# Kernel tuning notes

Hardware: AMD Instinct MI355X
Metric: run time of the kernel (lower is better)

The kernel has to match this reference:

```python
import jax, jax.numpy as jnp
import numpy as np

B, H, W, C = 16, 32, 32, 512
L, CT = 77, 512
NH, HD = 8, 64
G = 32          # GroupNorm groups
EPS = 1e-6      # flax GroupNorm default epsilon
NEG = -1e10


def group_norm(x, scale, bias):
    # flax GroupNorm on [b, n, c]: stats over (n, channels-within-group) per (b, group)
    b, n, c = x.shape
    xg = x.reshape(b, n, G, c // G)
    mu = xg.mean(axis=(1, 3), keepdims=True)
    var = xg.var(axis=(1, 3), keepdims=True)
    xg = (xg - mu) * jax.lax.rsqrt(var + EPS)
    return xg.reshape(b, n, c) * scale + bias


def setup_inputs() -> dict:
    key = jax.random.key(0)
    ks = jax.random.split(key, 8)
    w = lambda k, shape: jax.random.normal(k, shape, jnp.float32) * 0.02
    return {
        "inputs": jax.random.normal(ks[0], (B, H, W, C), jnp.float32),
        "text_enc": jax.random.normal(ks[1], (B, L, CT), jnp.float32),
        "text_mask": jnp.ones((B, L), jnp.int32),
        "gn_q_scale": jnp.ones((C,), jnp.float32),
        "gn_q_bias": jnp.zeros((C,), jnp.float32),
        "gn_kv_scale": jnp.ones((C,), jnp.float32),
        "gn_kv_bias": jnp.zeros((C,), jnp.float32),
        "gn_t_scale": jnp.ones((CT,), jnp.float32),
        "gn_t_bias": jnp.zeros((CT,), jnp.float32),
        "Wq": w(ks[2], (C, NH, HD)),
        "Wk_self": w(ks[3], (C, NH, HD)),
        "Wv_self": w(ks[4], (C, NH, HD)),
        "Wk_cross": w(ks[5], (CT, NH, HD)),
        "Wv_cross": w(ks[6], (CT, NH, HD)),
        "Wout": w(ks[7], (NH, HD, C)),
    }


def reference(inputs, text_enc, text_mask,
              gn_q_scale, gn_q_bias, gn_kv_scale, gn_kv_bias,
              gn_t_scale, gn_t_bias,
              Wq, Wk_self, Wv_self, Wk_cross, Wv_cross, Wout):
    b, h, w, c = inputs.shape
    n = h * w
    x = inputs.reshape(b, n, c)

    x_q = group_norm(x, gn_q_scale, gn_q_bias)
    x_kv = group_norm(x, gn_kv_scale, gn_kv_bias)
    t = group_norm(text_enc, gn_t_scale, gn_t_bias)

    # q/k/v projections; fused: KV = concat(self-KV from image, cross-KV from text)
    scale = jnp.asarray(1.0 / np.sqrt(HD), inputs.dtype)
    q = jnp.einsum('bqc,chd->bqhd', x_q, Wq) * scale  # scale_attn_logits
    k = jnp.concatenate([jnp.einsum('bkc,chd->bkhd', x_kv, Wk_self),
                         jnp.einsum('blc,chd->blhd', t, Wk_cross)], axis=1)
    v = jnp.concatenate([jnp.einsum('bkc,chd->bkhd', x_kv, Wv_self),
                         jnp.einsum('blc,chd->blhd', t, Wv_cross)], axis=1)

    # make_attention_mask(ones[b,n], concat(ones[b,n], text_mask)) -> [b,1,n,n+l];
    # query mask is all ones so only the KV mask matters.
    kv_mask = jnp.concatenate(
        [jnp.ones((b, n), jnp.bool_), text_mask > 0], axis=1)  # [b, n+l]

    logits = jnp.einsum('bqhd,bkhd->bhqk', q, k)  # [b, nh, n, n+l]
    logits = jnp.where(kv_mask[:, None, None, :], logits, jnp.asarray(NEG, logits.dtype))
    probs = jax.nn.softmax(logits, axis=-1)
    attn = jnp.einsum('bhqk,bkhd->bqhd', probs, v)
    out = jnp.einsum('bqhd,hdc->bqc', attn, Wout)
    return out.reshape(b, h, w, c) + inputs
```

## Files before the change

kernel.cpp:

```cpp
#include <hip/hip_runtime.h>
#include <hip/hip_bf16.h>

typedef __hip_bfloat16 bf16;
typedef __attribute__((ext_vector_type(8))) short short8;
typedef __attribute__((ext_vector_type(4))) float f32x4;
typedef __attribute__((ext_vector_type(16))) float f32x16;
#define MFMA16(a, b, c) __builtin_amdgcn_mfma_f32_16x16x32_bf16(a, b, c, 0, 0, 0)
#define MFMA32(a, b, c) __builtin_amdgcn_mfma_f32_32x32x16_bf16(a, b, c, 0, 0, 0)

#define BB   16
#define CCH  512
#define NN   1024
#define LLT  77
#define LPAD 128
#define NHH  8
#define HDD  64
#define GGN  32
#define NKV  1101
#define KVP  1152

__device__ __forceinline__ unsigned short f2bu(float f){
  bf16 h = __float2bfloat16(f);
  return *reinterpret_cast<unsigned short*>(&h);
}

__device__ __forceinline__ unsigned pk2(float lo, float hi){
  unsigned r;
  asm("v_cvt_pk_bf16_f32 %0, %1, %2" : "=v"(r) : "v"(lo), "v"(hi));
  return r;
}

__device__ __forceinline__ float fexp2(float x){
  float r;
  asm("v_exp_f32 %0, %1" : "=v"(r) : "v"(x));
  return r;
}

__device__ __forceinline__ void pl32swap(unsigned &a, unsigned &b){
  asm("v_permlane32_swap_b32 %0, %1" : "+v"(a), "+v"(b));
}

__device__ __forceinline__ void gload16(const bf16* g, bf16* l){
  __builtin_amdgcn_global_load_lds(
      (const __attribute__((address_space(1))) unsigned int*)g,
      (__attribute__((address_space(3))) unsigned int*)l,
      16, 0, 0);
}

__global__ __launch_bounds__(256) void pre_kernel(
    const float* __restrict__ ximg, const float* __restrict__ xtxt,
    float* __restrict__ stats,
    const float* __restrict__ W0, const float* __restrict__ W1,
    const float* __restrict__ W2, const float* __restrict__ W3,
    const float* __restrict__ W4, const float* __restrict__ W5,
    bf16* __restrict__ Wt)
{
  __shared__ float sh1[256], sh2[256];
  __shared__ alignas(16) float Ws[64][68];

  if (blockIdx.x < 1024){
    int isimg = blockIdx.x < 512;
    int bid = blockIdx.x & 511;
    int b = bid >> 5, g = bid & 31;
    int npos = isimg ? NN : LLT;
    const float* xb = (isimg ? ximg : xtxt) + (size_t)b * npos * CCH + g * 16;
    int tot4 = npos * 4;
    float s = 0.f, s2 = 0.f;
    for (int e = threadIdx.x; e < tot4; e += 256){
      int n = e >> 2, cq = (e & 3) * 4;
      float4 v = *(const float4*)(xb + (size_t)n * CCH + cq);
      s  += v.x + v.y + v.z + v.w;
      s2 += v.x * v.x + v.y * v.y + v.z * v.z + v.w * v.w;
    }
    sh1[threadIdx.x] = s; sh2[threadIdx.x] = s2;
    __syncthreads();
    for (int off = 128; off > 0; off >>= 1){
      if (threadIdx.x < off){
        sh1[threadIdx.x] += sh1[threadIdx.x + off];
        sh2[threadIdx.x] += sh2[threadIdx.x + off];
      }
      __syncthreads();
    }
    if (threadIdx.x == 0){
      float inv = 1.f / (float)(npos * 16);
      float m = sh1[0] * inv;
      float var = sh2[0] * inv - m * m;
      float* mu = stats + (isimg ? 0 : 1024);
      mu[bid] = m;
      mu[512 + bid] = rsqrtf(var + 1e-6f);
    }
  } else {
    int i = blockIdx.x - 1024;
    int wsel = i >> 6;
    int rem  = i & 63;
    int n0 = (rem & 7) * 64, k0 = (rem >> 3) * 64;
    const float* W = wsel == 0 ? W0 : wsel == 1 ? W1 : wsel == 2 ? W2 :
                     wsel == 3 ? W3 : wsel == 4 ? W4 : W5;
    bf16* dst = Wt + (size_t)wsel * CCH * CCH;

    int r = threadIdx.x >> 2, c = (threadIdx.x & 3) * 16;
    const float* src = W + (size_t)(k0 + r) * CCH + n0 + c;
    *(float4*)&Ws[r][c]      = *(const float4*)(src);
    *(float4*)&Ws[r][c + 4]  = *(const float4*)(src + 4);
    *(float4*)&Ws[r][c + 8]  = *(const float4*)(src + 8);
    *(float4*)&Ws[r][c + 12] = *(const float4*)(src + 12);
    __syncthreads();

    int nr = threadIdx.x >> 2, kc = (threadIdx.x & 3) * 16;
    uint4 o0, o1;
    o0.x = pk2(Ws[kc + 0][nr],  Ws[kc + 1][nr]);
    o0.y = pk2(Ws[kc + 2][nr],  Ws[kc + 3][nr]);
    o0.z = pk2(Ws[kc + 4][nr],  Ws[kc + 5][nr]);
    o0.w = pk2(Ws[kc + 6][nr],  Ws[kc + 7][nr]);
    o1.x = pk2(Ws[kc + 8][nr],  Ws[kc + 9][nr]);
    o1.y = pk2(Ws[kc + 10][nr], Ws[kc + 11][nr]);
    o1.z = pk2(Ws[kc + 12][nr], Ws[kc + 13][nr]);
    o1.w = pk2(Ws[kc + 14][nr], Ws[kc + 15][nr]);
    bf16* d = dst + (size_t)(n0 + nr) * CCH + k0 + kc;
    *(uint4*)d = o0;
    *(uint4*)(d + 8) = o1;
  }
}

__global__ __launch_bounds__(256) void norm_all_kernel(
    const float* __restrict__ x, const float* __restrict__ t,
    const float* __restrict__ stats,
    const float* __restrict__ gqs, const float* __restrict__ gqb,
    const float* __restrict__ gks, const float* __restrict__ gkb,
    const float* __restrict__ gts, const float* __restrict__ gtb,
    bf16* __restrict__ Xq, bf16* __restrict__ Xkv, bf16* __restrict__ Tn)
{
  if (blockIdx.x < 4096){
    size_t e = ((size_t)blockIdx.x * 256 + threadIdx.x) * 8;
    int b  = (int)(e >> 19);
    int ch = (int)(e & 511);
    int g  = ch >> 4;
    float m = stats[b * GGN + g], r = stats[512 + b * GGN + g];
    float4 x0 = *(const float4*)(x + e);
    float4 x1 = *(const float4*)(x + e + 4);
    float4 sq0 = *(const float4*)(gqs + ch), sq1 = *(const float4*)(gqs + ch + 4);
    float4 bq0 = *(const float4*)(gqb + ch), bq1 = *(const float4*)(gqb + ch + 4);
    float4 sk0 = *(const float4*)(gks + ch), sk1 = *(const float4*)(gks + ch + 4);
    float4 bk0 = *(const float4*)(gkb + ch), bk1 = *(const float4*)(gkb + ch + 4);
    float xs[8] = {x0.x,x0.y,x0.z,x0.w,x1.x,x1.y,x1.z,x1.w};
    float sqv[8] = {sq0.x,sq0.y,sq0.z,sq0.w,sq1.x,sq1.y,sq1.z,sq1.w};
    float bqv[8] = {bq0.x,bq0.y,bq0.z,bq0.w,bq1.x,bq1.y,bq1.z,bq1.w};
    float skv[8] = {sk0.x,sk0.y,sk0.z,sk0.w,sk1.x,sk1.y,sk1.z,sk1.w};
    float bkv[8] = {bk0.x,bk0.y,bk0.z,bk0.w,bk1.x,bk1.y,bk1.z,bk1.w};
    float q[8], k[8];
    #pragma unroll
    for (int j = 0; j < 8; j++){
      float nx = (xs[j] - m) * r;
      q[j] = (nx * sqv[j] + bqv[j]) * 0.18033688f;
      k[j] = nx * skv[j] + bkv[j];
    }
    uint4 oq, ok;
    oq.x = pk2(q[0], q[1]); oq.y = pk2(q[2], q[3]);
    oq.z = pk2(q[4], q[5]); oq.w = pk2(q[6], q[7]);
    ok.x = pk2(k[0], k[1]); ok.y = pk2(k[2], k[3]);
    ok.z = pk2(k[4], k[5]); ok.w = pk2(k[6], k[7]);
    *(uint4*)(Xq + e)  = oq;
    *(uint4*)(Xkv + e) = ok;
  } else {
    size_t e = ((size_t)(blockIdx.x - 4096) * 256 + threadIdx.x) * 8;
    int b  = (int)(e >> 16);
    int rem = (int)(e & 65535);
    int l  = rem >> 9;
    int ch = rem & 511;
    uint4 o;
    if (l < LLT){
      int g = ch >> 4;
      float m = stats[1024 + b * GGN + g], r = stats[1536 + b * GGN + g];
      const float* src = t + ((size_t)b * LLT + l) * CCH + ch;
      float4 x0 = *(const float4*)src, x1 = *(const float4*)(src + 4);
      float4 s0 = *(const float4*)(gts + ch), s1 = *(const float4*)(gts + ch + 4);
      float4 b0 = *(const float4*)(gtb + ch), b1 = *(const float4*)(gtb + ch + 4);
      float xs[8] = {x0.x,x0.y,x0.z,x0.w,x1.x,x1.y,x1.z,x1.w};
      float sv[8] = {s0.x,s0.y,s0.z,s0.w,s1.x,s1.y,s1.z,s1.w};
      float bv[8] = {b0.x,b0.y,b0.z,b0.w,b1.x,b1.y,b1.z,b1.w};
      float w[8];
      #pragma unroll
      for (int j = 0; j < 8; j++) w[j] = (xs[j] - m) * r * sv[j] + bv[j];
      o.x = pk2(w[0], w[1]); o.y = pk2(w[2], w[3]);
      o.z = pk2(w[4], w[5]); o.w = pk2(w[6], w[7]);
    } else {
      o = make_uint4(0, 0, 0, 0);
    }
    *(uint4*)(Tn + e) = o;
  }
}

__global__ __launch_bounds__(256) void proj_all_mfma(
    const bf16* __restrict__ Xq, const bf16* __restrict__ Xkv,
    const bf16* __restrict__ Tn, const bf16* __restrict__ Wt,
    bf16* __restrict__ Qo, bf16* __restrict__ Ko, bf16* __restrict__ Vo)
{
  __shared__ alignas(16) char SHRAW[36864];
  const int tid  = threadIdx.x;
  const int wave = tid >> 6, lane = tid & 63;
  const int l16 = lane & 15, quad = lane >> 4;
  const int bx = blockIdx.x;

  if (bx < 1536){
    bf16 (*T)[64][64] = reinterpret_cast<bf16(*)[64][64]>(SHRAW);
    const int wr = wave >> 1, wc = wave & 1;
    const int ct = bx >> 7;
    const int rt = bx & 127;
    const int mat = ct >> 2;
    const int cm0 = (ct & 3) * 128;
    const int b  = rt >> 3;
    const int n0 = (rt & 7) * 128;

    const bf16* A  = (mat == 0) ? Xq : Xkv;
    const bf16* Bw = Wt + (size_t)mat * CCH * CCH + (size_t)cm0 * CCH;

    f32x4 acc[4][4];
    #pragma unroll
    for (int rf = 0; rf < 4; rf++)
      #pragma unroll
      for (int cf = 0; cf < 4; cf++) acc[rf][cf] = (f32x4){0.f,0.f,0.f,0.f};

    const int lrow = lane >> 3, lcol = (lane & 7) * 8;
    const bf16* srcbase = (wave < 2)
        ? A  + ((size_t)b * NN + n0 + wave * 64) * CCH
        : Bw + (size_t)((wave - 2) * 64) * CCH;

    for (int kt = 0; kt < 8; kt++){
      const int kc = kt * 64;
      #pragma unroll
      for (int c = 0; c < 8; c++){
        const bf16* g = srcbase + (size_t)(c * 8 + lrow) * CCH + kc + lcol;
        gload16(g, &T[wave][c * 8][0]);
      }
      __syncthreads();

      short8 af[4][2];
      #pragma unroll
      for (int rf = 0; rf < 4; rf++){
        af[rf][0] = *(const short8*)&T[wr][rf * 16 + l16][quad * 8];
        af[rf][1] = *(const short8*)&T[wr][rf * 16 + l16][32 + quad * 8];
      }
      #pragma unroll
      for (int cf = 0; cf < 4; cf++){
        const short8 b0 = *(const short8*)&T[2 + wc][cf * 16 + l16][quad * 8];
        const short8 b1 = *(const short8*)&T[2 + wc][cf * 16 + l16][32 + quad * 8];
        #pragma unroll
        for (int rf = 0; rf < 4; rf++){
          acc[rf][cf] = MFMA16(af[rf][0], b0, acc[rf][cf]);
          acc[rf][cf] = MFMA16(af[rf][1], b1, acc[rf][cf]);
        }
      }
      __syncthreads();
    }

    if (mat < 2){
      bf16* Out = (mat == 0) ? Qo : Ko;
      const int stride = (mat == 0) ? NN : KVP;
      #pragma unroll
      for (int cf = 0; cf < 4; cf++){
        const int cm = cm0 + wc * 64 + cf * 16 + l16;
        const int h = cm >> 6, d = cm & 63;
        #pragma unroll
        for (int rf = 0; rf < 4; rf++)
          #pragma unroll
          for (int r = 0; r < 4; r++){
            const int n = n0 + wr * 64 + rf * 16 + quad * 4 + r;
            Out[(((size_t)b * NHH + h) * stride + n) * HDD + d] =
                __float2bfloat16(acc[rf][cf][r]);
          }
      }
    } else {
      bf16 (*Tw)[64] = T[wave];
      #pragma unroll
      for (int cf = 0; cf < 4; cf++)
        #pragma unroll
        for (int rf = 0; rf < 4; rf++)
          #pragma unroll
          for (int r = 0; r < 4; r++)
            Tw[cf * 16 + l16][rf * 16 + quad * 4 + r] =
                __float2bfloat16(acc[rf][cf][r]);
      __syncthreads();
      const int h  = (cm0 + wc * 64) >> 6;
      const int nb = n0 + wr * 64;
      const int dl = lane >> 2, cseg = (lane & 3) * 16;
      #pragma unroll
      for (int k2 = 0; k2 < 4; k2++){
        const int d = dl + k2 * 16;
        bf16* vd = Vo + (((size_t)b * NHH + h) * HDD + d) * KVP + nb + cseg;
        *(uint4*)vd       = *(const uint4*)&Tw[d][cseg];
        *(uint4*)(vd + 8) = *(const uint4*)&Tw[d][cseg + 8];
      }
    }
  } else {
    bf16 (*At)[72] = reinterpret_cast<bf16(*)[72]>(SHRAW);
    bf16 (*Bk)[72] = reinterpret_cast<bf16(*)[72]>(SHRAW + 64 * 72 * 2);
    bf16 (*Bv)[72] = reinterpret_cast<bf16(*)[72]>(SHRAW + 2 * 64 * 72 * 2);
    const int i  = bx - 1536;
    const int h  = i & 7;
    const int l0 = ((i >> 3) & 1) * 64;
    const int b  = i >> 4;

    const bf16* Wkc = Wt + 3 * CCH * CCH;
    const bf16* Wvc = Wt + 4 * CCH * CCH;

    f32x4 sk[4], sv[4];
    #pragma unroll
    for (int nt = 0; nt < 4; nt++){
      sk[nt] = (f32x4){0.f,0.f,0.f,0.f};
      sv[nt] = (f32x4){0.f,0.f,0.f,0.f};
    }

    const int sr = tid >> 2, sc = (tid & 3) * 16;
    const bf16* p_a  = Tn  + ((size_t)b * LPAD + l0 + sr) * CCH + sc;
    const bf16* p_bk = Wkc + (size_t)(h * 64 + sr) * CCH + sc;
    const bf16* p_bv = Wvc + (size_t)(h * 64 + sr) * CCH + sc;

    uint4 ra0 = *(const uint4*)p_a,   ra1 = *(const uint4*)(p_a + 8);
    uint4 rk0 = *(const uint4*)p_bk,  rk1 = *(const uint4*)(p_bk + 8);
    uint4 rv0 = *(const uint4*)p_bv,  rv1 = *(const uint4*)(p_bv + 8);

    for (int kt = 0; kt < 8; kt++){
      *(uint4*)&At[sr][sc]     = ra0;  *(uint4*)&At[sr][sc + 8] = ra1;
      *(uint4*)&Bk[sr][sc]     = rk0;  *(uint4*)&Bk[sr][sc + 8] = rk1;
      *(uint4*)&Bv[sr][sc]     = rv0;  *(uint4*)&Bv[sr][sc + 8] = rv1;
      if (kt < 7){
        const int k1 = (kt + 1) * 64;
        ra0 = *(const uint4*)(p_a + k1);   ra1 = *(const uint4*)(p_a + k1 + 8);
        rk0 = *(const uint4*)(p_bk + k1);  rk1 = *(const uint4*)(p_bk + k1 + 8);
        rv0 = *(const uint4*)(p_bv + k1);  rv1 = *(const uint4*)(p_bv + k1 + 8);
      }
      __syncthreads();

      const short8 a0 = *(const short8*)&At[wave * 16 + l16][quad * 8];
      const short8 a1 = *(const short8*)&At[wave * 16 + l16][32 + quad * 8];
      #pragma unroll
      for (int nt = 0; nt < 4; nt++){
        const short8 bk0 = *(const short8*)&Bk[nt * 16 + l16][quad * 8];
        const short8 bk1 = *(const short8*)&Bk[nt * 16 + l16][32 + quad * 8];
        sk[nt] = MFMA16(a0, bk0, sk[nt]);
        sk[nt] = MFMA16(a1, bk1, sk[nt]);
        const short8 bv0 = *(const short8*)&Bv[nt * 16 + l16][quad * 8];
        const short8 bv1 = *(const short8*)&Bv[nt * 16 + l16][32 + quad * 8];
        sv[nt] = MFMA16(a0, bv0, sv[nt]);
        sv[nt] = MFMA16(a1, bv1, sv[nt]);
      }
      __syncthreads();
    }

    #pragma unroll
    for (int r = 0; r < 4; r++){
      int kvrow = NN + l0 + wave * 16 + quad * 4 + r;
      bf16* kd = Ko + (((size_t)b * NHH + h) * KVP + kvrow) * HDD + l16;
      #pragma unroll
      for (int nt = 0; nt < 4; nt++)
        kd[nt * 16] = __float2bfloat16(sk[nt][r]);
    }

    __syncthreads();
    #pragma unroll
    for (int nt = 0; nt < 4; nt++)
      #pragma unroll
      for (int r = 0; r < 4; r++)
        Bk[nt * 16 + l16][wave * 16 + quad * 4 + r] = __float2bfloat16(sv[nt][r]);
    __syncthreads();
    {
      int d = tid >> 2, c = (tid & 3) * 16;
      bf16* vd = Vo + (((size_t)b * NHH + h) * HDD + d) * KVP + NN + l0 + c;
      *(uint4*)vd       = *(const uint4*)&Bk[d][c];
      *(uint4*)(vd + 8) = *(const uint4*)&Bk[d][c + 8];
    }
  }
}

__global__ __launch_bounds__(256, 4) void attn_mfma_kernel(
    const bf16* __restrict__ Q, const bf16* __restrict__ K,
    const bf16* __restrict__ Vt, const int* __restrict__ tmask,
    bf16* __restrict__ Ao)
{
  const int tid  = threadIdx.x;
  const int wave = tid >> 6;
  const int lane = tid & 63;
  const int l31  = lane & 31;
  const int hi   = lane >> 5;
  const int bx = blockIdx.x;
  const int q0 = (bx >> 7) * 128;
  const int g  = bx & 127;
  const int h  = g & 7;
  const int b  = g >> 3;

  __shared__ alignas(16) bf16 KV[2][2][64][72];

  const bf16* qp = Q + (((size_t)b * NHH + h) * NN + q0 + wave * 32 + l31) * HDD + hi * 8;
  short8 qf[4];
  qf[0] = *(const short8*)(qp);
  qf[1] = *(const short8*)(qp + 16);
  qf[2] = *(const short8*)(qp + 32);
  qf[3] = *(const short8*)(qp + 48);

  union { unsigned u[4]; short8 s8; } ones;
  ones.u[0] = 0x3F803F80u; ones.u[1] = 0x3F803F80u;
  ones.u[2] = 0x3F803F80u; ones.u[3] = 0x3F803F80u;

  f32x16 zf;
  #pragma unroll
  for (int i = 0; i < 16; i++) zf[i] = 0.f;

  f32x16 o_acc[2], l_acc;
  #pragma unroll
  for (int dt = 0; dt < 2; dt++)
    #pragma unroll
    for (int i = 0; i < 16; i++) o_acc[dt][i] = 0.f;
  #pragma unroll
  for (int i = 0; i < 16; i++) l_acc[i] = 0.f;

  const size_t kbase = ((size_t)b * NHH + h) * KVP;
  const size_t vbase = ((size_t)b * NHH + h) * (size_t)HDD * KVP;

  const int sr = tid >> 2;
  const int sc = (tid & 3) * 16;
  const bf16* kp = K  + (kbase + sr) * HDD + sc;
  const bf16* vp = Vt + vbase + (size_t)sr * KVP + sc;

  uint4 kr0 = *(const uint4*)kp, kr1 = *(const uint4*)(kp + 8);
  uint4 vr0 = *(const uint4*)vp, vr1 = *(const uint4*)(vp + 8);
  *(uint4*)&KV[0][0][sr][sc]     = kr0;
  *(uint4*)&KV[0][0][sr][sc + 8] = kr1;
  *(uint4*)&KV[0][1][sr][sc]     = vr0;
  *(uint4*)&KV[0][1][sr][sc + 8] = vr1;
  kr0 = *(const uint4*)(kp + 4096); kr1 = *(const uint4*)(kp + 4096 + 8);
  vr0 = *(const uint4*)(vp + 64);   vr1 = *(const uint4*)(vp + 64 + 8);
  __syncthreads();

  for (int kt = 0; kt < 18; kt++){
    const int cur = kt & 1;
    if (kt + 1 < 18){
      *(uint4*)&KV[cur ^ 1][0][sr][sc]     = kr0;
      *(uint4*)&KV[cur ^ 1][0][sr][sc + 8] = kr1;
      *(uint4*)&KV[cur ^ 1][1][sr][sc]     = vr0;
      *(uint4*)&KV[cur ^ 1][1][sr][sc + 8] = vr1;
    }
    if (kt + 2 < 18){
      const size_t ko = (size_t)(kt + 2) * 4096;
      const int    vo = (kt + 2) * 64;
      kr0 = *(const uint4*)(kp + ko); kr1 = *(const uint4*)(kp + ko + 8);
      vr0 = *(const uint4*)(vp + vo); vr1 = *(const uint4*)(vp + vo + 8);
    }

    const bf16 (*Ks)[72] = KV[cur][0];
    const bf16 (*Vs)[72] = KV[cur][1];
    const int kv0 = kt * 64;

    #pragma unroll
    for (int t = 0; t < 2; t++){
      const short8 kf0 = *(const short8*)&Ks[t * 32 + l31][hi * 8];
      const short8 kf1 = *(const short8*)&Ks[t * 32 + l31][16 + hi * 8];
      const short8 kf2 = *(const short8*)&Ks[t * 32 + l31][32 + hi * 8];
      const short8 kf3 = *(const short8*)&Ks[t * 32 + l31][48 + hi * 8];
      __builtin_amdgcn_s_setprio(1);
      f32x16 s = MFMA32(kf0, qf[0], zf);
      s = MFMA32(kf1, qf[1], s);
      s = MFMA32(kf2, qf[2], s);
      s = MFMA32(kf3, qf[3], s);
      __builtin_amdgcn_s_setprio(0);

      if (kv0 + 64 > NN){
        #pragma unroll
        for (int r = 0; r < 16; r++){
          int idx = kv0 - NN + t * 32 + (r & 3) + 8 * (r >> 2) + 4 * hi;
          int ci = idx < LLT ? idx : LLT - 1;
          float rep = (idx < LLT)
                        ? (tmask[b * LLT + ci] > 0 ? 1e30f : -1e10f)
                        : -1e30f;
          s[r] = fminf(s[r], rep);
        }
      }

      #pragma unroll
      for (int r = 0; r < 16; r++) s[r] = fexp2(s[r]);

      unsigned w0 = pk2(s[0],  s[1]),  w1 = pk2(s[2],  s[3]);
      unsigned w2 = pk2(s[4],  s[5]),  w3 = pk2(s[6],  s[7]);
      unsigned w4 = pk2(s[8],  s[9]),  w5 = pk2(s[10], s[11]);
      unsigned w6 = pk2(s[12], s[13]), w7 = pk2(s[14], s[15]);
      pl32swap(w0, w2);
      pl32swap(w1, w3);
      pl32swap(w4, w6);
      pl32swap(w5, w7);
      union { unsigned u[4]; short8 s8; } pf0, pf1;
      pf0.u[0] = w0; pf0.u[1] = w1; pf0.u[2] = w2; pf0.u[3] = w3;
      pf1.u[0] = w4; pf1.u[1] = w5; pf1.u[2] = w6; pf1.u[3] = w7;

      const short8 vf00 = *(const short8*)&Vs[l31][t * 32 + hi * 8];
      const short8 vf01 = *(const short8*)&Vs[l31][t * 32 + 16 + hi * 8];
      const short8 vf10 = *(const short8*)&Vs[32 + l31][t * 32 + hi * 8];
      const short8 vf11 = *(const short8*)&Vs[32 + l31][t * 32 + 16 + hi * 8];

      __builtin_amdgcn_s_setprio(1);
      l_acc = MFMA32(pf0.s8, ones.s8, l_acc);
      l_acc = MFMA32(pf1.s8, ones.s8, l_acc);
      o_acc[0] = MFMA32(pf0.s8, vf00, o_acc[0]);
      o_acc[0] = MFMA32(pf1.s8, vf01, o_acc[0]);
      o_acc[1] = MFMA32(pf0.s8, vf10, o_acc[1]);
      o_acc[1] = MFMA32(pf1.s8, vf11, o_acc[1]);
      __builtin_amdgcn_s_setprio(0);
    }
    __syncthreads();
  }

  #pragma unroll
  for (int r = 0; r < 16; r++){
    const int ql = (r & 3) + 8 * (r >> 2) + 4 * hi;
    const float linv = 1.f / l_acc[r];
    const int n = q0 + wave * 32 + ql;
    bf16* dst = Ao + ((size_t)b * NN + n) * CCH + h * HDD + l31;
    dst[0]  = __float2bfloat16(o_acc[0][r] * linv);
    dst[32] = __float2bfloat16(o_acc[1][r] * linv);
  }
}

__global__ __launch_bounds__(256) void outproj_mfma(
    const bf16* __restrict__ A, const bf16* __restrict__ Wt,
    const float* __restrict__ resid, float* __restrict__ out)
{
  __shared__ alignas(16) bf16 T[4][64][64];
  const int tid  = threadIdx.x;
  const int wave = tid >> 6, lane = tid & 63;
  const int l16 = lane & 15, quad = lane >> 4;
  const int wr = wave >> 1, wc = wave & 1;
  const int bx = blockIdx.x;
  const int c0 = (bx >> 7) * 128;
  const int g0 = (bx & 127) * 128;

  const bf16* Bw = Wt + (size_t)5 * CCH * CCH + (size_t)c0 * CCH;

  f32x4 acc[4][4];
  #pragma unroll
  for (int rf = 0; rf < 4; rf++)
    #pragma unroll
    for (int cf = 0; cf < 4; cf++) acc[rf][cf] = (f32x4){0.f,0.f,0.f,0.f};

  const int lrow = lane >> 3, lcol = (lane & 7) * 8;
  const bf16* srcbase = (wave < 2)
      ? A  + ((size_t)g0 + wave * 64) * CCH
      : Bw + (size_t)((wave - 2) * 64) * CCH;

  for (int kt = 0; kt < 8; kt++){
    const int kc = kt * 64;
    #pragma unroll
    for (int c = 0; c < 8; c++){
      const bf16* g = srcbase + (size_t)(c * 8 + lrow) * CCH + kc + lcol;
      gload16(g, &T[wave][c * 8][0]);
    }
    __syncthreads();

    short8 af[4][2];
    #pragma unroll
    for (int rf = 0; rf < 4; rf++){
      af[rf][0] = *(const short8*)&T[wr][rf * 16 + l16][quad * 8];
      af[rf][1] = *(const short8*)&T[wr][rf * 16 + l16][32 + quad * 8];
    }
    #pragma unroll
    for (int cf = 0; cf < 4; cf++){
      const short8 b0 = *(const short8*)&T[2 + wc][cf * 16 + l16][quad * 8];
      const short8 b1 = *(const short8*)&T[2 + wc][cf * 16 + l16][32 + quad * 8];
      #pragma unroll
      for (int rf = 0; rf < 4; rf++){
        acc[rf][cf] = MFMA16(af[rf][0], b0, acc[rf][cf]);
        acc[rf][cf] = MFMA16(af[rf][1], b1, acc[rf][cf]);
      }
    }
    __syncthreads();
  }

  #pragma unroll
  for (int rf = 0; rf < 4; rf++)
    #pragma unroll
    for (int r = 0; r < 4; r++){
      const size_t row = (size_t)g0 + wr * 64 + rf * 16 + quad * 4 + r;
      #pragma unroll
      for (int cf = 0; cf < 4; cf++){
        const int col = c0 + wc * 64 + cf * 16 + l16;
        out[row * CCH + col] = acc[rf][cf][r] + resid[row * CCH + col];
      }
    }
}

extern "C" void kernel_launch(void* const* d_in, const int* in_sizes, int n_in,
                              void* d_out, int out_size, void* d_ws, size_t ws_size,
                              hipStream_t stream)
{
  const float* x     = (const float*)d_in[0];
  const float* txt   = (const float*)d_in[1];
  const int*   tmask = (const int*)d_in[2];
  const float* gqs   = (const float*)d_in[3];
  const float* gqb   = (const float*)d_in[4];
  const float* gks   = (const float*)d_in[5];
  const float* gkb   = (const float*)d_in[6];
  const float* gts   = (const float*)d_in[7];
  const float* gtb   = (const float*)d_in[8];
  const float* Wq    = (const float*)d_in[9];
  const float* Wks   = (const float*)d_in[10];
  const float* Wvs   = (const float*)d_in[11];
  const float* Wkc   = (const float*)d_in[12];
  const float* Wvc   = (const float*)d_in[13];
  const float* Wout  = (const float*)d_in[14];

  float* stats = (float*)d_ws;
  bf16* WtAll = (bf16*)(stats + 2048);
  bf16* Xq  = WtAll + (size_t)6 * CCH * CCH;
  bf16* Xkv = Xq  + (size_t)BB * NN * CCH;
  bf16* Tn  = Xkv + (size_t)BB * NN * CCH;
  bf16* Qw  = Tn  + (size_t)BB * LPAD * CCH;
  bf16* Kw  = Qw  + (size_t)BB * NHH * NN * HDD;
  bf16* Vw  = Kw  + (size_t)BB * NHH * KVP * HDD;
  bf16* Aw  = Xq;

  pre_kernel<<<1408, 256, 0, stream>>>(
      x, txt, stats, Wq, Wks, Wvs, Wkc, Wvc, Wout, WtAll);
  norm_all_kernel<<<4608, 256, 0, stream>>>(
      x, txt, stats, gqs, gqb, gks, gkb, gts, gtb, Xq, Xkv, Tn);
  proj_all_mfma<<<1792, 256, 0, stream>>>(
      Xq, Xkv, Tn, WtAll, Qw, Kw, Vw);
  attn_mfma_kernel<<<1024, 256, 0, stream>>>(Qw, Kw, Vw, tmask, Aw);
  outproj_mfma<<<512, 256, 0, stream>>>(Aw, WtAll, x, (float*)d_out);
}
```

Baseline: 241.9 us.

## Fuse self K and V projections into one block sharing the Xkv tile

```diff
diff --git a/kernel.cpp b/kernel.cpp
--- a/kernel.cpp
+++ b/kernel.cpp
@@ -195,24 +195,23 @@
     const bf16* __restrict__ Tn, const bf16* __restrict__ Wt,
     bf16* __restrict__ Qo, bf16* __restrict__ Ko, bf16* __restrict__ Vo)
 {
-  __shared__ alignas(16) char SHRAW[36864];
+  __shared__ alignas(16) char SHRAW[49152];
   const int tid  = threadIdx.x;
   const int wave = tid >> 6, lane = tid & 63;
   const int l16 = lane & 15, quad = lane >> 4;
   const int bx = blockIdx.x;
-
-  if (bx < 1536){
+  const int lrow = lane >> 3, lcol = (lane & 7) * 8;
+
+  if (bx < 512){
     bf16 (*T)[64][64] = reinterpret_cast<bf16(*)[64][64]>(SHRAW);
     const int wr = wave >> 1, wc = wave & 1;
     const int ct = bx >> 7;
     const int rt = bx & 127;
-    const int mat = ct >> 2;
-    const int cm0 = (ct & 3) * 128;
+    const int cm0 = ct * 128;
     const int b  = rt >> 3;
     const int n0 = (rt & 7) * 128;
 
-    const bf16* A  = (mat == 0) ? Xq : Xkv;
-    const bf16* Bw = Wt + (size_t)mat * CCH * CCH + (size_t)cm0 * CCH;
+    const bf16* Bw = Wt + (size_t)cm0 * CCH;
 
     f32x4 acc[4][4];
     #pragma unroll
@@ -220,9 +219,8 @@
       #pragma unroll
       for (int cf = 0; cf < 4; cf++) acc[rf][cf] = (f32x4){0.f,0.f,0.f,0.f};
 
-    const int lrow = lane >> 3, lcol = (lane & 7) * 8;
     const bf16* srcbase = (wave < 2)
-        ? A  + ((size_t)b * NN + n0 + wave * 64) * CCH
+        ? Xq + ((size_t)b * NN + n0 + wave * 64) * CCH
         : Bw + (size_t)((wave - 2) * 64) * CCH;
 
     for (int kt = 0; kt < 8; kt++){
@@ -253,35 +251,121 @@
       __syncthreads();
     }
 
-    if (mat < 2){
-      bf16* Out = (mat == 0) ? Qo : Ko;
-      const int stride = (mat == 0) ? NN : KVP;
-      #pragma unroll
-      for (int cf = 0; cf < 4; cf++){
-        const int cm = cm0 + wc * 64 + cf * 16 + l16;
-        const int h = cm >> 6, d = cm & 63;
-        #pragma unroll
-        for (int rf = 0; rf < 4; rf++)
-          #pragma unroll
-          for (int r = 0; r < 4; r++){
-            const int n = n0 + wr * 64 + rf * 16 + quad * 4 + r;
-            Out[(((size_t)b * NHH + h) * stride + n) * HDD + d] =
-                __float2bfloat16(acc[rf][cf][r]);
-          }
-      }
-    } else {
-      bf16 (*Tw)[64] = T[wave];
+    bf16 (*Tw)[64] = T[wave];
+    #pragma unroll
+    for (int rf = 0; rf < 4; rf++)
       #pragma unroll
       for (int cf = 0; cf < 4; cf++)
         #pragma unroll
-        for (int rf = 0; rf < 4; rf++)
-          #pragma unroll
-          for (int r = 0; r < 4; r++)
-            Tw[cf * 16 + l16][rf * 16 + quad * 4 + r] =
-                __float2bfloat16(acc[rf][cf][r]);
+        for (int r = 0; r < 4; r++)
+          Tw[rf * 16 + quad * 4 + r][cf * 16 + l16] =
+              __float2bfloat16(acc[rf][cf][r]);
+    const int h  = (cm0 + wc * 64) >> 6;
+    const int nb = n0 + wr * 64;
+    const int rr = lane >> 2, cs = (lane & 3) * 16;
+    #pragma unroll
+    for (int k2 = 0; k2 < 4; k2++){
+      const int row = rr + k2 * 16;
+      bf16* qd = Qo + (((size_t)b * NHH + h) * NN + nb + row) * HDD + cs;
+      *(uint4*)qd       = *(const uint4*)&Tw[row][cs];
+      *(uint4*)(qd + 8) = *(const uint4*)&Tw[row][cs + 8];
+    }
+  } else if (bx < 1024){
+    bf16 (*T)[64][64] = reinterpret_cast<bf16(*)[64][64]>(SHRAW);
+    const int wr = wave >> 1, wc = wave & 1;
+    const int ct = (bx - 512) >> 7;
+    const int rt = bx & 127;
+    const int cm0 = ct * 128;
+    const int b  = rt >> 3;
+    const int n0 = (rt & 7) * 128;
+
+    const bf16* Bk_ = Wt + 1 * (size_t)CCH * CCH + (size_t)cm0 * CCH;
+    const bf16* Bv_ = Wt + 2 * (size_t)CCH * CCH + (size_t)cm0 * CCH;
+
+    f32x4 aK[4][4], aV[4][4];
+    #pragma unroll
+    for (int rf = 0; rf < 4; rf++)
+      #pragma unroll
+      for (int cf = 0; cf < 4; cf++){
+        aK[rf][cf] = (f32x4){0.f,0.f,0.f,0.f};
+        aV[rf][cf] = (f32x4){0.f,0.f,0.f,0.f};
+      }
+
+    for (int kt = 0; kt < 8; kt++){
+      const int kc = kt * 64;
+      #pragma unroll
+      for (int j = 0; j < 12; j++){
+        const int i = wave * 12 + j;
+        const int tile = i >> 3, ch = i & 7;
+        const bf16* base;
+        if (tile < 2)      base = Xkv + ((size_t)b * NN + n0 + tile * 64) * CCH;
+        else if (tile < 4) base = Bk_ + (size_t)((tile - 2) * 64) * CCH;
+        else               base = Bv_ + (size_t)((tile - 4) * 64) * CCH;
+        const bf16* g = base + (size_t)(ch * 8 + lrow) * CCH + kc + lcol;
+        gload16(g, &T[tile][ch * 8][0]);
+      }
       __syncthreads();
-      const int h  = (cm0 + wc * 64) >> 6;
-      const int nb = n0 + wr * 64;
+
+      short8 af[4][2];
+      #pragma unroll
+      for (int rf = 0; rf < 4; rf++){
+        af[rf][0] = *(const short8*)&T[wr][rf * 16 + l16][quad * 8];
+        af[rf][1] = *(const short8*)&T[wr][rf * 16 + l16][32 + quad * 8];
+      }
+      #pragma unroll
+      for (int cf = 0; cf < 4; cf++){
+        const short8 bk0 = *(const short8*)&T[2 + wc][cf * 16 + l16][quad * 8];
+        const short8 bk1 = *(const short8*)&T[2 + wc][cf * 16 + l16][32 + quad * 8];
+        #pragma unroll
+        for (int rf = 0; rf < 4; rf++){
+          aK[rf][cf] = MFMA16(af[rf][0], bk0, aK[rf][cf]);
+          aK[rf][cf] = MFMA16(af[rf][1], bk1, aK[rf][cf]);
+        }
+        const short8 bv0 = *(const short8*)&T[4 + wc][cf * 16 + l16][quad * 8];
+        const short8 bv1 = *(const short8*)&T[4 + wc][cf * 16 + l16][32 + quad * 8];
+        #pragma unroll
+        for (int rf = 0; rf < 4; rf++){
+          aV[rf][cf] = MFMA16(af[rf][0], bv0, aV[rf][cf]);
+          aV[rf][cf] = MFMA16(af[rf][1], bv1, aV[rf][cf]);
+        }
+      }
+      __syncthreads();
+    }
+
+    const int h  = (cm0 + wc * 64) >> 6;
+    const int nb = n0 + wr * 64;
+    bf16 (*Tw)[64] = T[wave];
+
+    #pragma unroll
+    for (int rf = 0; rf < 4; rf++)
+      #pragma unroll
+      for (int cf = 0; cf < 4; cf++)
+        #pragma unroll
+        for (int r = 0; r < 4; r++)
+          Tw[rf * 16 + quad * 4 + r][cf * 16 + l16] =
+              __float2bfloat16(aK[rf][cf][r]);
+    {
+      const int rr = lane >> 2, cs = (lane & 3) * 16;
+      #pragma unroll
+      for (int k2 = 0; k2 < 4; k2++){
+        const int row = rr + k2 * 16;
+        bf16* kd = Ko + (((size_t)b * NHH + h) * KVP + nb + row) * HDD + cs;
+        *(uint4*)kd       = *(const uint4*)&Tw[row][cs];
+        *(uint4*)(kd + 8) = *(const uint4*)&Tw[row][cs + 8];
+      }
+    }
+    __syncthreads();
+
+    #pragma unroll
+    for (int cf = 0; cf < 4; cf++)
+      #pragma unroll
+      for (int rf = 0; rf < 4; rf++)
+        #pragma unroll
+        for (int r = 0; r < 4; r++)
+          Tw[cf * 16 + l16][rf * 16 + quad * 4 + r] =
+              __float2bfloat16(aV[rf][cf][r]);
+    __syncthreads();
+    {
       const int dl = lane >> 2, cseg = (lane & 3) * 16;
       #pragma unroll
       for (int k2 = 0; k2 < 4; k2++){
@@ -295,13 +379,13 @@
     bf16 (*At)[72] = reinterpret_cast<bf16(*)[72]>(SHRAW);
     bf16 (*Bk)[72] = reinterpret_cast<bf16(*)[72]>(SHRAW + 64 * 72 * 2);
     bf16 (*Bv)[72] = reinterpret_cast<bf16(*)[72]>(SHRAW + 2 * 64 * 72 * 2);
-    const int i  = bx - 1536;
+    const int i  = bx - 1024;
     const int h  = i & 7;
     const int l0 = ((i >> 3) & 1) * 64;
     const int b  = i >> 4;
 
-    const bf16* Wkc = Wt + 3 * CCH * CCH;
-    const bf16* Wvc = Wt + 4 * CCH * CCH;
+    const bf16* Wkc = Wt + 3 * (size_t)CCH * CCH;
+    const bf16* Wvc = Wt + 4 * (size_t)CCH * CCH;
 
     f32x4 sk[4], sv[4];
     #pragma unroll
@@ -619,7 +703,7 @@
       x, txt, stats, Wq, Wks, Wvs, Wkc, Wvc, Wout, WtAll);
   norm_all_kernel<<<4608, 256, 0, stream>>>(
       x, txt, stats, gqs, gqb, gks, gkb, gts, gtb, Xq, Xkv, Tn);
-  proj_all_mfma<<<1792, 256, 0, stream>>>(
+  proj_all_mfma<<<1280, 256, 0, stream>>>(
       Xq, Xkv, Tn, WtAll, Qw, Kw, Vw);
   attn_mfma_kernel<<<1024, 256, 0, stream>>>(Qw, Kw, Vw, tmask, Aw);
   outproj_mfma<<<512, 256, 0, stream>>>(Aw, WtAll, x, (float*)d_out);
```

Result: slower. 265.2 us (+9.6%).
